# Optimization experiments

Measured on AMD Instinct MI355X. Metric: run time of the kernel, lower is better.

Reference implementation:

```python
import jax, jax.numpy as jnp
import numpy as np
from functools import partial

D_MODEL, N_HEADS, D_FF, KSIZE = 512, 8, 2048, 31
B, S = 8, 1024
EPS = 1e-5

def layer_norm(x, g, b):
    m = jnp.mean(x, axis=-1, keepdims=True)
    v = jnp.mean(jnp.square(x - m), axis=-1, keepdims=True)
    return (x - m) * jax.lax.rsqrt(v + EPS) * g + b

def ffn(x, ln_g, ln_b, w1, b1, w2, b2):
    h = layer_norm(x, ln_g, ln_b)
    h = jax.nn.silu(h @ w1 + b1) @ w2 + b2
    return x + 0.5 * h

def mhsa(x, ln_g, ln_b, wq, bq, wk, bk, wv, bv, wo, bo):
    b_, s_, d_ = x.shape
    dk = d_ // N_HEADS
    h = layer_norm(x, ln_g, ln_b)
    def heads(y):  # (B,S,D) -> (B,H,S,dk)
        return y.reshape(b_, s_, N_HEADS, dk).transpose(0, 2, 1, 3)
    Q, K, V = heads(h @ wq + bq), heads(h @ wk + bk), heads(h @ wv + bv)
    scores = jnp.einsum('bhqd,bhkd->bhqk', Q, K) / jnp.sqrt(jnp.float32(dk)).astype(x.dtype)
    attn = jax.nn.softmax(scores, axis=-1)
    ctx = jnp.einsum('bhqk,bhkd->bhqd', attn, V)
    ctx = ctx.transpose(0, 2, 1, 3).reshape(b_, s_, d_)
    return x + (ctx @ wo + bo)

def conv_module(x, ln_g, ln_b, pw1_w, pw1_b, dw_w, dw_b, bn_g, bn_b, bn_mean, bn_var, pw2_w, pw2_b):
    h = layer_norm(x, ln_g, ln_b)           # (B,S,D)
    h = h @ pw1_w + pw1_b                   # (B,S,2D) pointwise conv1 (k=1)
    a, g = jnp.split(h, 2, axis=-1)
    h = a * jax.nn.sigmoid(g)               # GLU over channel dim
    hc = h.transpose(0, 2, 1)               # (B,D,S)
    # depthwise conv: kernel (D,1,K), groups=D, SAME padding (K odd)
    hc = jax.lax.conv_general_dilated(
        hc, dw_w, window_strides=(1,), padding='SAME',
        dimension_numbers=('NCH', 'OIH', 'NCH'),
        feature_group_count=D_MODEL) + dw_b[None, :, None]
    # BatchNorm1d (eval mode, running stats)
    hc = (hc - bn_mean[None, :, None]) * jax.lax.rsqrt(bn_var + EPS)[None, :, None]
    hc = hc * bn_g[None, :, None] + bn_b[None, :, None]
    hc = jax.nn.silu(hc)
    hc = jnp.einsum('bcs,co->bos', hc, pw2_w) + pw2_b[None, :, None]  # pointwise conv2
    return x + hc.transpose(0, 2, 1)


def setup_inputs() -> dict:
    key = jax.random.key(0)
    ks = iter(jax.random.split(key, 48))
    def w(shape, scale=0.02):
        return (jax.random.normal(next(ks), shape, dtype=jnp.float32) * scale)
    d, f = D_MODEL, D_FF
    inp = {
        'x': jax.random.normal(next(ks), (B, S, d), dtype=jnp.float32),
        # FFN1
        'ffn1_ln_g': jnp.ones((d,)), 'ffn1_ln_b': jnp.zeros((d,)),
        'ffn1_w1': w((d, f)), 'ffn1_b1': jnp.zeros((f,)),
        'ffn1_w2': w((f, d)), 'ffn1_b2': jnp.zeros((d,)),
        # MHSA
        'mhsa_ln_g': jnp.ones((d,)), 'mhsa_ln_b': jnp.zeros((d,)),
        'wq': w((d, d)), 'bq': jnp.zeros((d,)),
        'wk': w((d, d)), 'bk': jnp.zeros((d,)),
        'wv': w((d, d)), 'bv': jnp.zeros((d,)),
        'wo': w((d, d)), 'bo': jnp.zeros((d,)),
        # Conv module
        'conv_ln_g': jnp.ones((d,)), 'conv_ln_b': jnp.zeros((d,)),
        'pw1_w': w((d, 2 * d)), 'pw1_b': jnp.zeros((2 * d,)),
        'dw_w': w((d, 1, KSIZE)), 'dw_b': jnp.zeros((d,)),
        'bn_g': jnp.ones((d,)), 'bn_b': jnp.zeros((d,)),
        'bn_mean': jnp.zeros((d,)), 'bn_var': jnp.ones((d,)),
        'pw2_w': w((d, d)), 'pw2_b': jnp.zeros((d,)),
        # FFN2
        'ffn2_ln_g': jnp.ones((d,)), 'ffn2_ln_b': jnp.zeros((d,)),
        'ffn2_w1': w((d, f)), 'ffn2_b1': jnp.zeros((f,)),
        'ffn2_w2': w((f, d)), 'ffn2_b2': jnp.zeros((d,)),
        # Final LN
        'final_ln_g': jnp.ones((d,)), 'final_ln_b': jnp.zeros((d,)),
    }
    return inp


def reference(x,
              ffn1_ln_g, ffn1_ln_b, ffn1_w1, ffn1_b1, ffn1_w2, ffn1_b2,
              mhsa_ln_g, mhsa_ln_b, wq, bq, wk, bk, wv, bv, wo, bo,
              conv_ln_g, conv_ln_b, pw1_w, pw1_b, dw_w, dw_b,
              bn_g, bn_b, bn_mean, bn_var, pw2_w, pw2_b,
              ffn2_ln_g, ffn2_ln_b, ffn2_w1, ffn2_b1, ffn2_w2, ffn2_b2,
              final_ln_g, final_ln_b):
    h = ffn(x, ffn1_ln_g, ffn1_ln_b, ffn1_w1, ffn1_b1, ffn1_w2, ffn1_b2)
    h = mhsa(h, mhsa_ln_g, mhsa_ln_b, wq, bq, wk, bk, wv, bv, wo, bo)
    h = conv_module(h, conv_ln_g, conv_ln_b, pw1_w, pw1_b, dw_w, dw_b,
                    bn_g, bn_b, bn_mean, bn_var, pw2_w, pw2_b)
    h = ffn(h, ffn2_ln_g, ffn2_ln_b, ffn2_w1, ffn2_b1, ffn2_w2, ffn2_b2)
    return layer_norm(h, final_ln_g, final_ln_b)
```

## Files before the change

### kernel.cpp

```cpp
#include <hip/hip_runtime.h>
#include <hip/hip_bf16.h>
#include <cstddef>

typedef __hip_bfloat16 bf16;
typedef __attribute__((ext_vector_type(8))) short bf16x8;
typedef __attribute__((ext_vector_type(4))) float f32x4;
typedef __attribute__((ext_vector_type(2))) unsigned int u32x2;

static __device__ __forceinline__ float b2f(bf16 v) { return __bfloat162float(v); }
static __device__ __forceinline__ bf16 f2b(float v) { return __float2bfloat16(v); }
static __device__ __forceinline__ float bits2f(unsigned short u) {
    union { unsigned int i; float f; } c; c.i = ((unsigned int)u) << 16; return c.f;
}
static __device__ __forceinline__ unsigned int f2bu(float v) {
    union { bf16 b; unsigned short u; } c; c.b = f2b(v); return (unsigned int)c.u;
}
static __device__ __forceinline__ float ldx(const void* p, size_t i, bool isbf) {
    return isbf ? b2f(((const bf16*)p)[i]) : ((const float*)p)[i];
}
#define GLOAD_LDS16(g, l)                                                            \
    __builtin_amdgcn_global_load_lds((const __attribute__((address_space(1))) unsigned int*)(g), \
                                     (__attribute__((address_space(3))) unsigned int*)(l), 16, 0, 0)

#define LN_EPS 1e-5f

__global__ void detect_kernel(const void* ones, int* flag) {
    unsigned int w = *(const unsigned int*)ones;
    *flag = (w == 0x3F803F80u) ? 1 : 0;
}

__global__ __launch_bounds__(256) void ln_init_kernel(const void* __restrict__ X,
                                                      const void* __restrict__ g,
                                                      const void* __restrict__ b,
                                                      float* __restrict__ res,
                                                      bf16* __restrict__ O, const int* flag) {
    bool isbf = (*flag != 0);
    int tid = threadIdx.x, lane = tid & 63, wid = tid >> 6;
    int t = blockIdx.x * 4 + wid;
    size_t off = (size_t)t * 512 + lane * 8;
    __attribute__((aligned(16))) float v[8];
    if (isbf) {
        bf16x8 xv = *(const bf16x8*)((const bf16*)X + off);
#pragma unroll
        for (int u = 0; u < 8; ++u) v[u] = bits2f((unsigned short)xv[u]);
    } else {
        *(f32x4*)&v[0] = *(const f32x4*)((const float*)X + off);
        *(f32x4*)&v[4] = *(const f32x4*)((const float*)X + off + 4);
    }
    *(f32x4*)(res + off) = *(f32x4*)&v[0];
    *(f32x4*)(res + off + 4) = *(f32x4*)&v[4];
    float s = 0.f, q = 0.f;
#pragma unroll
    for (int u = 0; u < 8; ++u) { s += v[u]; q += v[u] * v[u]; }
#pragma unroll
    for (int m = 1; m < 64; m <<= 1) { s += __shfl_xor(s, m, 64); q += __shfl_xor(q, m, 64); }
    float mean = s * (1.f / 512.f);
    float var  = q * (1.f / 512.f) - mean * mean;
    float sc = rsqrtf(var + LN_EPS);
    __attribute__((aligned(16))) bf16 ov[8];
#pragma unroll
    for (int u = 0; u < 8; ++u)
        ov[u] = f2b((v[u] - mean) * sc * ldx(g, lane * 8 + u, isbf) + ldx(b, lane * 8 + u, isbf));
    *(bf16x8*)(O + off) = *(bf16x8*)ov;
}

__global__ __launch_bounds__(256) void transpose_kernel(const void* __restrict__ W,
                                                        bf16* __restrict__ Wt,
                                                        int K, int M, const int* flag) {
    bool isbf = (*flag != 0);
    __shared__ float ts[32][33];
    int kt0 = blockIdx.x * 32, mt0 = blockIdx.y * 32;
    int x = threadIdx.x, y = threadIdx.y;
    for (int yy = y; yy < 32; yy += 8)
        ts[yy][x] = ldx(W, (size_t)(kt0 + yy) * M + mt0 + x, isbf);
    __syncthreads();
    for (int yy = y; yy < 32; yy += 8)
        Wt[(size_t)(mt0 + yy) * K + kt0 + x] = f2b(ts[x][yy]);
}

__global__ __launch_bounds__(256) void glutrans_kernel(const void* __restrict__ W,
                                                       bf16* __restrict__ Wt, const int* flag) {
    bool isbf = (*flag != 0);
    __shared__ float ts[32][33];
    int kt0 = blockIdx.x * 32, mt0 = blockIdx.y * 32;
    int x = threadIdx.x, y = threadIdx.y;
    for (int yy = y; yy < 32; yy += 8)
        ts[yy][x] = ldx(W, (size_t)(kt0 + yy) * 1024 + mt0 + x, isbf);
    __syncthreads();
    for (int yy = y; yy < 32; yy += 8) {
        int c = mt0 + yy;
        int p = (c < 512) ? (2 * c) : (2 * (c - 512) + 1);
        Wt[(size_t)p * 512 + kt0 + x] = f2b(ts[x][yy]);
    }
}

__global__ void glubias_kernel(const void* __restrict__ b, float* __restrict__ out,
                               const int* flag) {
    bool isbf = (*flag != 0);
    int p = blockIdx.x * blockDim.x + threadIdx.x;
    if (p >= 1024) return;
    int c = (p & 1) ? (p >> 1) + 512 : (p >> 1);
    out[p] = ldx(b, c, isbf);
}

__global__ void bpack_kernel(const void* bq, const void* bk, const void* bv,
                             void* out, const int* flag) {
    bool isbf = (*flag != 0);
    int i = blockIdx.x * blockDim.x + threadIdx.x;
    if (i >= 1536) return;
    const void* src = (i < 512) ? bq : ((i < 1024) ? bk : bv);
    float v = ldx(src, i & 511, isbf);
    if (isbf) ((bf16*)out)[i] = f2b(v);
    else      ((float*)out)[i] = v;
}

__global__ __launch_bounds__(256) void ln_kernel(const float* __restrict__ X,
                                                 const void* __restrict__ g,
                                                 const void* __restrict__ b,
                                                 bf16* __restrict__ O, const int* flag) {
    bool isbf = (*flag != 0);
    int tid = threadIdx.x, lane = tid & 63, wid = tid >> 6;
    int t = blockIdx.x * 4 + wid;
    const float* x = X + (size_t)t * 512 + lane * 8;
    __attribute__((aligned(16))) float v[8];
    *(f32x4*)&v[0] = *(const f32x4*)x;
    *(f32x4*)&v[4] = *(const f32x4*)(x + 4);
    float s = 0.f, q = 0.f;
#pragma unroll
    for (int u = 0; u < 8; ++u) { s += v[u]; q += v[u] * v[u]; }
#pragma unroll
    for (int m = 1; m < 64; m <<= 1) { s += __shfl_xor(s, m, 64); q += __shfl_xor(q, m, 64); }
    float mean = s * (1.f / 512.f);
    float var  = q * (1.f / 512.f) - mean * mean;
    float sc = rsqrtf(var + LN_EPS);
    __attribute__((aligned(16))) bf16 ov[8];
#pragma unroll
    for (int u = 0; u < 8; ++u)
        ov[u] = f2b((v[u] - mean) * sc * ldx(g, lane * 8 + u, isbf) + ldx(b, lane * 8 + u, isbf));
    *(bf16x8*)(O + (size_t)t * 512 + lane * 8) = *(bf16x8*)ov;
}

__global__ __launch_bounds__(256) void ln_out_kernel(const float* __restrict__ X,
                                                     const void* __restrict__ g,
                                                     const void* __restrict__ b,
                                                     void* __restrict__ O, const int* flag) {
    bool isbf = (*flag != 0);
    int tid = threadIdx.x, lane = tid & 63, wid = tid >> 6;
    int t = blockIdx.x * 4 + wid;
    const float* x = X + (size_t)t * 512 + lane * 8;
    __attribute__((aligned(16))) float v[8];
    *(f32x4*)&v[0] = *(const f32x4*)x;
    *(f32x4*)&v[4] = *(const f32x4*)(x + 4);
    float s = 0.f, q = 0.f;
#pragma unroll
    for (int u = 0; u < 8; ++u) { s += v[u]; q += v[u] * v[u]; }
#pragma unroll
    for (int m = 1; m < 64; m <<= 1) { s += __shfl_xor(s, m, 64); q += __shfl_xor(q, m, 64); }
    float mean = s * (1.f / 512.f);
    float var  = q * (1.f / 512.f) - mean * mean;
    float sc = rsqrtf(var + LN_EPS);
    float r[8];
#pragma unroll
    for (int u = 0; u < 8; ++u)
        r[u] = (v[u] - mean) * sc * ldx(g, lane * 8 + u, isbf) + ldx(b, lane * 8 + u, isbf);
    size_t off = (size_t)t * 512 + lane * 8;
    if (isbf) {
        __attribute__((aligned(16))) bf16 ov[8];
#pragma unroll
        for (int u = 0; u < 8; ++u) ov[u] = f2b(r[u]);
        *(bf16x8*)((bf16*)O + off) = *(bf16x8*)ov;
    } else {
        *(f32x4*)((float*)O + off) = *(f32x4*)&r[0];
        *(f32x4*)((float*)O + off + 4) = *(f32x4*)&r[4];
    }
}

template <int ACT, int RESADD, int BM, int MODE>
__global__ __launch_bounds__(256) void mgemm_kernel(const bf16* __restrict__ A,
                                                    const bf16* __restrict__ Wt,
                                                    const void* __restrict__ bias,
                                                    bf16* __restrict__ Cb,
                                                    bf16* __restrict__ vt,
                                                    float* __restrict__ res, float alpha,
                                                    int lda, int K, int M, const int* flag) {
    constexpr int MI = BM / 32;
    bool isbf = (*flag != 0);
    __shared__ short smem[2 * BM * 64 + 2 * 128 * 64];
    short (*As)[BM * 64]  = (short(*)[BM * 64])smem;
    short (*Bs)[128 * 64] = (short(*)[128 * 64])(smem + 2 * BM * 64);
    int tid = threadIdx.x;
    int gx = gridDim.x;
    int nwg = gx * gridDim.y;
    int flat = blockIdx.y * gx + blockIdx.x;
    if ((nwg & 7) == 0) { int cpx = nwg >> 3; flat = (flat & 7) * cpx + (flat >> 3); }
    int rowBase = (flat / gx) * BM, colBase = (flat % gx) * 128;
    int ll = tid & 63, wv = tid >> 6;
    int wr = (wv & 1) * (BM / 2), wc = (wv >> 1) * 64;
    int lRow = ll & 15, quad = ll >> 4;
    int rr = ll >> 3;
    int ch = (ll & 7) ^ rr;
    int slA = (quad ^ (lRow & 7)) * 8;

    int nSteps = K >> 6;

    f32x4 acc[MI][4] = {};

    auto STAGE = [&](int buf, int k0) {
#pragma unroll
        for (int j = 0; j < MI; ++j) {
            int rT = wv * (BM / 4) + j * 8;
            const bf16* ga = A + (size_t)(rowBase + rT + rr) * lda + k0 + ch * 8;
            GLOAD_LDS16(ga, &As[buf][rT * 64]);
        }
#pragma unroll
        for (int j = 0; j < 4; ++j) {
            int rT = wv * 32 + j * 8;
            const bf16* gb = Wt + (size_t)(colBase + rT + rr) * K + k0 + ch * 8;
            GLOAD_LDS16(gb, &Bs[buf][rT * 64]);
        }
    };

    STAGE(0, 0);
    STAGE(1, 64);
    if constexpr (BM == 128) asm volatile("s_waitcnt vmcnt(8)" ::: "memory");
    else                     asm volatile("s_waitcnt vmcnt(6)" ::: "memory");
    __builtin_amdgcn_s_barrier();

    for (int it = 0; it < nSteps; ++it) {
        int cur = it & 1;
        const short* Ac = &As[cur][0];
        const short* Bc = &Bs[cur][0];
        bf16x8 af[2][MI], bfv[2][4];
#pragma unroll
        for (int h = 0; h < 2; ++h) {
            int sl = slA ^ (h * 32);
#pragma unroll
            for (int i = 0; i < MI; ++i)
                af[h][i] = *(const bf16x8*)&Ac[(wr + i * 16 + lRow) * 64 + sl];
#pragma unroll
            for (int j = 0; j < 4; ++j)
                bfv[h][j] = *(const bf16x8*)&Bc[(wc + j * 16 + lRow) * 64 + sl];
        }
        asm volatile("s_waitcnt lgkmcnt(0)" ::: "memory");
        __builtin_amdgcn_s_barrier();
        bool pf = (it + 2 < nSteps);
        if (pf) STAGE(cur, (it + 2) * 64);
#pragma unroll
        for (int h = 0; h < 2; ++h)
#pragma unroll
            for (int i = 0; i < MI; ++i)
#pragma unroll
                for (int j = 0; j < 4; ++j) {
                    if constexpr (MODE == 1)
                        acc[i][j] = __builtin_amdgcn_mfma_f32_16x16x32_bf16(bfv[h][j], af[h][i], acc[i][j], 0, 0, 0);
                    else
                        acc[i][j] = __builtin_amdgcn_mfma_f32_16x16x32_bf16(af[h][i], bfv[h][j], acc[i][j], 0, 0, 0);
                }
        if (pf) {
            if constexpr (BM == 128) asm volatile("s_waitcnt vmcnt(8)" ::: "memory");
            else                     asm volatile("s_waitcnt vmcnt(6)" ::: "memory");
        } else {
            asm volatile("s_waitcnt vmcnt(0)" ::: "memory");
        }
        __builtin_amdgcn_s_barrier();
    }

    if constexpr (MODE == 1) {
        const float* bI = (const float*)bias;
#pragma unroll
        for (int j = 0; j < 4; ++j) {
            int colB = colBase + wc + j * 16 + quad * 4;
            float b0 = bI[colB], b1 = bI[colB + 1], b2 = bI[colB + 2], b3 = bI[colB + 3];
#pragma unroll
            for (int i = 0; i < MI; ++i) {
                int row = rowBase + wr + i * 16 + lRow;
                float a0 = acc[i][j][0] + b0, g0 = acc[i][j][1] + b1;
                float a1 = acc[i][j][2] + b2, g1 = acc[i][j][3] + b3;
                float o0 = a0 / (1.f + __expf(-g0));
                float o1 = a1 / (1.f + __expf(-g1));
                union { bf16 b2_[2]; unsigned int w; } ou;
                ou.b2_[0] = f2b(o0); ou.b2_[1] = f2b(o1);
                *(unsigned int*)(Cb + (size_t)row * (M / 2) + colB / 2) = ou.w;
            }
        }
        return;
    }

    if constexpr (MODE == 2) {
        if (colBase >= 1024) {
            short* T = smem;
#pragma unroll
            for (int j = 0; j < 4; ++j) {
                int colL = wc + j * 16 + lRow;
                float bv = ldx(bias, colBase + colL, isbf);
#pragma unroll
                for (int i = 0; i < MI; ++i) {
                    int r0L = wr + i * 16 + quad * 4;
                    union { bf16 b4[4]; u32x2 w; } ou;
#pragma unroll
                    for (int r = 0; r < 4; ++r) ou.b4[r] = f2b(acc[i][j][r] + bv);
                    *(u32x2*)&T[colL * 136 + r0L] = ou.w;
                }
            }
            __syncthreads();
            int c = tid >> 1, half = tid & 1;
            int cg = colBase - 1024 + c;
            bf16* dst = vt + (size_t)(rowBase >> 10) * 524288 + (size_t)cg * 1024 +
                        (rowBase & 1023) + half * 64;
#pragma unroll
            for (int k = 0; k < 8; ++k)
                *(bf16x8*)(dst + k * 8) = *(const bf16x8*)&T[c * 136 + half * 64 + k * 8];
            return;
        }
    }

#pragma unroll
    for (int j = 0; j < 4; ++j) {
        int col = colBase + wc + j * 16 + lRow;
        float bv = ldx(bias, col, isbf);
#pragma unroll
        for (int i = 0; i < MI; ++i) {
            int r0 = rowBase + wr + i * 16 + quad * 4;
#pragma unroll
            for (int r = 0; r < 4; ++r) {
                float v = acc[i][j][r] + bv;
                if (ACT == 1) v = v / (1.f + __expf(-v));
                int row = r0 + r;
                if (RESADD) res[(size_t)row * 512 + col] += alpha * v;
                else        Cb[(size_t)row * M + col] = f2b(v);
            }
        }
    }
}

__global__ __launch_bounds__(256) void fattn_kernel(bf16* __restrict__ QO,
                                                    const bf16* __restrict__ Vt) {
    __shared__ short Ks[2][64 * 64];
    __shared__ short Vs[2][64 * 64];
    int tid = threadIdx.x, wid = tid >> 6, ll = tid & 63;
    int n = ll & 15, quad = ll >> 4;
    int id = blockIdx.x;
    int ng = gridDim.x >> 3;
    int g = id % ng, j = id / ng;
    int h = g & 7, b = g >> 3;
    size_t rowB = (size_t)b * 1024;
    int q0 = j * 128 + wid * 32;

    const bf16* Qb = QO + rowB * 1536 + h * 64;
    bf16x8 qA0 = *(const bf16x8*)(Qb + (size_t)(q0 + n) * 1536 + quad * 8);
    bf16x8 qA1 = *(const bf16x8*)(Qb + (size_t)(q0 + n) * 1536 + 32 + quad * 8);
    bf16x8 qB0 = *(const bf16x8*)(Qb + (size_t)(q0 + 16 + n) * 1536 + quad * 8);
    bf16x8 qB1 = *(const bf16x8*)(Qb + (size_t)(q0 + 16 + n) * 1536 + 32 + quad * 8);

    const bf16* Kb = QO + rowB * 1536 + 512 + h * 64;
    const bf16* Vb = Vt + (size_t)b * 512 * 1024 + (size_t)(h * 64) * 1024;

    int rr = ll >> 3;
    int ch = (ll & 7) ^ rr;

    float la = 0.f, lb = 0.f;
    f32x4 oaccA0 = {}, oaccA1 = {}, oaccA2 = {}, oaccA3 = {};
    f32x4 oaccB0 = {}, oaccB1 = {}, oaccB2 = {}, oaccB3 = {};
    int idxA = (((quad & 1) * 32) + n) * 4;
    int idxB = idxA + 64;
    bool hiC = (quad >= 2);
    int nx = n & 7;
    int sl0 = (quad ^ nx) * 8;
    int sl1 = sl0 ^ (4 * 8);

    auto STAGE = [&](int buf, int k0) {
#pragma unroll
        for (int i2 = 0; i2 < 2; ++i2) {
            int r0 = wid * 16 + i2 * 8;
            const bf16* gk = Kb + (size_t)(k0 + r0 + rr) * 1536 + ch * 8;
            GLOAD_LDS16(gk, &Ks[buf][r0 * 64]);
            const bf16* gv = Vb + (size_t)(r0 + rr) * 1024 + k0 + ch * 8;
            GLOAD_LDS16(gv, &Vs[buf][r0 * 64]);
        }
    };

    auto COMPUTE = [&](const short* Kc, const short* Vc) {
#pragma unroll
        for (int s = 0; s < 2; ++s) {
            const short* kb0 = Kc + (s * 32 + n) * 64;
            const short* kb1 = kb0 + 16 * 64;
            bf16x8 k00 = *(const bf16x8*)(kb0 + sl0);
            bf16x8 k01 = *(const bf16x8*)(kb0 + sl1);
            bf16x8 k10 = *(const bf16x8*)(kb1 + sl0);
            bf16x8 k11 = *(const bf16x8*)(kb1 + sl1);
            f32x4 sA0 = {}, sA1 = {}, sB0 = {}, sB1 = {};
            sA0 = __builtin_amdgcn_mfma_f32_16x16x32_bf16(k00, qA0, sA0, 0, 0, 0);
            sA0 = __builtin_amdgcn_mfma_f32_16x16x32_bf16(k01, qA1, sA0, 0, 0, 0);
            sA1 = __builtin_amdgcn_mfma_f32_16x16x32_bf16(k10, qA0, sA1, 0, 0, 0);
            sA1 = __builtin_amdgcn_mfma_f32_16x16x32_bf16(k11, qA1, sA1, 0, 0, 0);
            sB0 = __builtin_amdgcn_mfma_f32_16x16x32_bf16(k00, qB0, sB0, 0, 0, 0);
            sB0 = __builtin_amdgcn_mfma_f32_16x16x32_bf16(k01, qB1, sB0, 0, 0, 0);
            sB1 = __builtin_amdgcn_mfma_f32_16x16x32_bf16(k10, qB0, sB1, 0, 0, 0);
            sB1 = __builtin_amdgcn_mfma_f32_16x16x32_bf16(k11, qB1, sB1, 0, 0, 0);

            float pA0[4], pA1[4], pB0[4], pB1[4];
#pragma unroll
            for (int r = 0; r < 4; ++r) {
                pA0[r] = __expf(sA0[r] * 0.125f);
                pA1[r] = __expf(sA1[r] * 0.125f);
                pB0[r] = __expf(sB0[r] * 0.125f);
                pB1[r] = __expf(sB1[r] * 0.125f);
                la += pA0[r] + pA1[r];
                lb += pB0[r] + pB1[r];
            }

            int A0d0 = (int)(f2bu(pA0[0]) | (f2bu(pA0[1]) << 16));
            int A0d1 = (int)(f2bu(pA0[2]) | (f2bu(pA0[3]) << 16));
            int A1d0 = (int)(f2bu(pA1[0]) | (f2bu(pA1[1]) << 16));
            int A1d1 = (int)(f2bu(pA1[2]) | (f2bu(pA1[3]) << 16));
            int B0d0 = (int)(f2bu(pB0[0]) | (f2bu(pB0[1]) << 16));
            int B0d1 = (int)(f2bu(pB0[2]) | (f2bu(pB0[3]) << 16));
            int B1d0 = (int)(f2bu(pB1[0]) | (f2bu(pB1[1]) << 16));
            int B1d1 = (int)(f2bu(pB1[2]) | (f2bu(pB1[3]) << 16));

            int aa0 = __builtin_amdgcn_ds_bpermute(idxA, A0d0);
            int aa1 = __builtin_amdgcn_ds_bpermute(idxA, A0d1);
            int aa2 = __builtin_amdgcn_ds_bpermute(idxB, A0d0);
            int aa3 = __builtin_amdgcn_ds_bpermute(idxB, A0d1);
            int ac0 = __builtin_amdgcn_ds_bpermute(idxA, A1d0);
            int ac1 = __builtin_amdgcn_ds_bpermute(idxA, A1d1);
            int ac2 = __builtin_amdgcn_ds_bpermute(idxB, A1d0);
            int ac3 = __builtin_amdgcn_ds_bpermute(idxB, A1d1);
            int ba0 = __builtin_amdgcn_ds_bpermute(idxA, B0d0);
            int ba1 = __builtin_amdgcn_ds_bpermute(idxA, B0d1);
            int ba2 = __builtin_amdgcn_ds_bpermute(idxB, B0d0);
            int ba3 = __builtin_amdgcn_ds_bpermute(idxB, B0d1);
            int bc0 = __builtin_amdgcn_ds_bpermute(idxA, B1d0);
            int bc1 = __builtin_amdgcn_ds_bpermute(idxA, B1d1);
            int bc2 = __builtin_amdgcn_ds_bpermute(idxB, B1d0);
            int bc3 = __builtin_amdgcn_ds_bpermute(idxB, B1d1);
            union { int d[4]; bf16x8 v; } bfA, bfB;
            bfA.d[0] = hiC ? ac0 : aa0;
            bfA.d[1] = hiC ? ac1 : aa1;
            bfA.d[2] = hiC ? ac2 : aa2;
            bfA.d[3] = hiC ? ac3 : aa3;
            bfB.d[0] = hiC ? bc0 : ba0;
            bfB.d[1] = hiC ? bc1 : ba1;
            bfB.d[2] = hiC ? bc2 : ba2;
            bfB.d[3] = hiC ? bc3 : ba3;

            int vsl = ((s * 4 + quad) ^ nx) * 8;
            bf16x8 v0 = *(const bf16x8*)(Vc + (0 * 16 + n) * 64 + vsl);
            bf16x8 v1 = *(const bf16x8*)(Vc + (1 * 16 + n) * 64 + vsl);
            bf16x8 v2 = *(const bf16x8*)(Vc + (2 * 16 + n) * 64 + vsl);
            bf16x8 v3 = *(const bf16x8*)(Vc + (3 * 16 + n) * 64 + vsl);
            oaccA0 = __builtin_amdgcn_mfma_f32_16x16x32_bf16(v0, bfA.v, oaccA0, 0, 0, 0);
            oaccB0 = __builtin_amdgcn_mfma_f32_16x16x32_bf16(v0, bfB.v, oaccB0, 0, 0, 0);
            oaccA1 = __builtin_amdgcn_mfma_f32_16x16x32_bf16(v1, bfA.v, oaccA1, 0, 0, 0);
            oaccB1 = __builtin_amdgcn_mfma_f32_16x16x32_bf16(v1, bfB.v, oaccB1, 0, 0, 0);
            oaccA2 = __builtin_amdgcn_mfma_f32_16x16x32_bf16(v2, bfA.v, oaccA2, 0, 0, 0);
            oaccB2 = __builtin_amdgcn_mfma_f32_16x16x32_bf16(v2, bfB.v, oaccB2, 0, 0, 0);
            oaccA3 = __builtin_amdgcn_mfma_f32_16x16x32_bf16(v3, bfA.v, oaccA3, 0, 0, 0);
            oaccB3 = __builtin_amdgcn_mfma_f32_16x16x32_bf16(v3, bfB.v, oaccB3, 0, 0, 0);
        }
    };

    STAGE(0, 0);
    __syncthreads();
    for (int it = 0; it < 16; it += 2) {
        if (it + 1 < 16) STAGE(1, (it + 1) * 64);
        COMPUTE(&Ks[0][0], &Vs[0][0]);
        __syncthreads();
        if (it + 2 < 16) STAGE(0, (it + 2) * 64);
        COMPUTE(&Ks[1][0], &Vs[1][0]);
        __syncthreads();
    }

    la += __shfl_xor(la, 16, 64);
    la += __shfl_xor(la, 32, 64);
    lb += __shfl_xor(lb, 16, 64);
    lb += __shfl_xor(lb, 32, 64);
    float linvA = 1.f / la;
    float linvB = 1.f / lb;
    bf16* opA = QO + (rowB + q0 + n) * 1536 + h * 64 + quad * 4;
    bf16* opB = QO + (rowB + q0 + 16 + n) * 1536 + h * 64 + quad * 4;
    {
        union { bf16 b4[4]; u32x2 w; } ou;
#pragma unroll
        for (int r = 0; r < 4; ++r) ou.b4[r] = f2b(oaccA0[r] * linvA);
        *(u32x2*)(opA + 0) = ou.w;
#pragma unroll
        for (int r = 0; r < 4; ++r) ou.b4[r] = f2b(oaccA1[r] * linvA);
        *(u32x2*)(opA + 16) = ou.w;
#pragma unroll
        for (int r = 0; r < 4; ++r) ou.b4[r] = f2b(oaccA2[r] * linvA);
        *(u32x2*)(opA + 32) = ou.w;
#pragma unroll
        for (int r = 0; r < 4; ++r) ou.b4[r] = f2b(oaccA3[r] * linvA);
        *(u32x2*)(opA + 48) = ou.w;
#pragma unroll
        for (int r = 0; r < 4; ++r) ou.b4[r] = f2b(oaccB0[r] * linvB);
        *(u32x2*)(opB + 0) = ou.w;
#pragma unroll
        for (int r = 0; r < 4; ++r) ou.b4[r] = f2b(oaccB1[r] * linvB);
        *(u32x2*)(opB + 16) = ou.w;
#pragma unroll
        for (int r = 0; r < 4; ++r) ou.b4[r] = f2b(oaccB2[r] * linvB);
        *(u32x2*)(opB + 32) = ou.w;
#pragma unroll
        for (int r = 0; r < 4; ++r) ou.b4[r] = f2b(oaccB3[r] * linvB);
        *(u32x2*)(opB + 48) = ou.w;
    }
}

__global__ void dwprep_kernel(const void* __restrict__ w, const void* __restrict__ dwb,
                              const void* __restrict__ bng, const void* __restrict__ bnb,
                              const void* __restrict__ bnm, const void* __restrict__ bnv,
                              bf16* __restrict__ wT, float* __restrict__ scl,
                              float* __restrict__ sft, const int* flag) {
    bool isbf = (*flag != 0);
    int c = blockIdx.x * blockDim.x + threadIdx.x;
    if (c >= 512) return;
    for (int k = 0; k < 31; ++k) wT[k * 512 + c] = f2b(ldx(w, (size_t)c * 31 + k, isbf));
    float s = ldx(bng, c, isbf) * rsqrtf(ldx(bnv, c, isbf) + LN_EPS);
    scl[c] = s;
    sft[c] = (ldx(dwb, c, isbf) - ldx(bnm, c, isbf)) * s + ldx(bnb, c, isbf);
}

__global__ __launch_bounds__(256) void dwconv_kernel(const bf16* __restrict__ X,
                                                     const bf16* __restrict__ wT,
                                                     const float* __restrict__ scl,
                                                     const float* __restrict__ sft,
                                                     bf16* __restrict__ Out) {
    __shared__ bf16 wl[31 * 512];
    __shared__ float sl[512], fl[512];
    int tid = threadIdx.x;
    for (int i = tid; i < (31 * 512) / 8; i += 256)
        *(bf16x8*)&wl[i * 8] = *(const bf16x8*)&wT[i * 8];
    sl[tid] = scl[tid]; sl[tid + 256] = scl[tid + 256];
    fl[tid] = sft[tid]; fl[tid + 256] = sft[tid + 256];
    __syncthreads();

    int lane = tid & 63, sg = tid >> 6;
    int c = lane * 8;
    size_t bOff = (size_t)blockIdx.y * 1024 * 512;
    int sb = blockIdx.x * 16 + sg * 4;

    float acc[4][8] = {};
    for (int kk = 0; kk < 34; ++kk) {
        int sp = sb + kk - 15;
        if (sp < 0 || sp >= 1024) continue;
        bf16x8 xr = *(const bf16x8*)(X + bOff + (size_t)sp * 512 + c);
        float xv[8];
#pragma unroll
        for (int u = 0; u < 8; ++u) xv[u] = bits2f((unsigned short)xr[u]);
#pragma unroll
        for (int o = 0; o < 4; ++o) {
            int kw = kk - o;
            if (kw < 0 || kw > 30) continue;
            bf16x8 wv8 = *(const bf16x8*)&wl[kw * 512 + c];
#pragma unroll
            for (int u = 0; u < 8; ++u) acc[o][u] += xv[u] * bits2f((unsigned short)wv8[u]);
        }
    }
#pragma unroll
    for (int o = 0; o < 4; ++o) {
        __attribute__((aligned(16))) bf16 ov[8];
#pragma unroll
        for (int u = 0; u < 8; ++u) {
            float v = acc[o][u] * sl[c + u] + fl[c + u];
            v = v / (1.f + __expf(-v));
            ov[u] = f2b(v);
        }
        *(bf16x8*)(Out + bOff + (size_t)(sb + o) * 512 + c) = *(bf16x8*)ov;
    }
}

extern "C" void kernel_launch(void* const* d_in, const int* in_sizes, int n_in,
                              void* d_out, int out_size, void* d_ws, size_t ws_size,
                              hipStream_t stream) {
    const int B = 8, S = 1024, D = 512, F = 2048, H = 8;
    const int N = B * S;
    const size_t ND = (size_t)N * D;
    if (n_in < 37) return;

    int idx = 0;
    const void* x          = d_in[idx++];
    const void* ffn1_ln_g  = d_in[idx++];
    const void* ffn1_ln_b  = d_in[idx++];
    const void* ffn1_w1    = d_in[idx++];
    const void* ffn1_b1    = d_in[idx++];
    const void* ffn1_w2    = d_in[idx++];
    const void* ffn1_b2    = d_in[idx++];
    const void* mhsa_ln_g  = d_in[idx++];
    const void* mhsa_ln_b  = d_in[idx++];
    const void* wq         = d_in[idx++];
    const void* bq         = d_in[idx++];
    const void* wk         = d_in[idx++];
    const void* bk         = d_in[idx++];
    const void* wv         = d_in[idx++];
    const void* bv         = d_in[idx++];
    const void* wo         = d_in[idx++];
    const void* bo         = d_in[idx++];
    const void* conv_ln_g  = d_in[idx++];
    const void* conv_ln_b  = d_in[idx++];
    const void* pw1_w      = d_in[idx++];
    const void* pw1_b      = d_in[idx++];
    const void* dw_w       = d_in[idx++];
    const void* dw_b       = d_in[idx++];
    const void* bn_g       = d_in[idx++];
    const void* bn_b       = d_in[idx++];
    const void* bn_mean    = d_in[idx++];
    const void* bn_var     = d_in[idx++];
    const void* pw2_w      = d_in[idx++];
    const void* pw2_b      = d_in[idx++];
    const void* ffn2_ln_g  = d_in[idx++];
    const void* ffn2_ln_b  = d_in[idx++];
    const void* ffn2_w1    = d_in[idx++];
    const void* ffn2_b1    = d_in[idx++];
    const void* ffn2_w2    = d_in[idx++];
    const void* ffn2_b2    = d_in[idx++];
    const void* final_ln_g = d_in[idx++];
    const void* final_ln_b = d_in[idx++];

    const size_t MB = 1024 * 1024;
    char* wsb  = (char*)d_ws;
    int*  flag = (int*)wsb;
    float* res = (float*)(wsb + 1024);
    bf16*  wt  = (bf16*)(wsb + 1024 + ND * 4);
    char*  dwr = wsb + 1024 + ND * 4 + 4 * MB;
    bf16*  dwT  = (bf16*)dwr;
    float* dscl = (float*)(dwr + 32768);
    float* dsft = dscl + 512;
    void*  qkvB = (void*)(dwr + 40960);
    float* gbias = (float*)(dwr + 49152);
    char*  scr = dwr + 65536;
    size_t base = 1024 + ND * 4 + 4 * MB + 65536;
    size_t scrB = (ws_size > base) ? ws_size - base : 0;
    int ffnRows = (scrB >= 32 * MB) ? 8192 : ((scrB >= 8 * MB) ? 2048 : 1024);
    int bI      = (scrB >= 32 * MB) ? 8    : ((scrB >= 8 * MB) ? 2    : 1);
    int cI      = (scrB >= 32 * MB) ? 8    : ((scrB >= 8 * MB) ? 2    : 1);

    bf16* h = (bf16*)d_out;

    detect_kernel<<<1, 1, 0, stream>>>(ffn1_ln_g, flag);
    ln_init_kernel<<<N / 4, 256, 0, stream>>>(x, ffn1_ln_g, ffn1_ln_b, res, h, flag);

    auto run_ffn = [&](const void* lg, const void* lb, const void* w1, const void* b1,
                       const void* w2, const void* b2, bool doLn) {
        bf16* w1t = wt;
        bf16* w2t = wt + (size_t)D * F;
        transpose_kernel<<<dim3(D / 32, F / 32), dim3(32, 8), 0, stream>>>(w1, w1t, D, F, flag);
        transpose_kernel<<<dim3(F / 32, D / 32), dim3(32, 8), 0, stream>>>(w2, w2t, F, D, flag);
        if (doLn) ln_kernel<<<N / 4, 256, 0, stream>>>(res, lg, lb, h, flag);
        bf16* mid = (bf16*)scr;
        for (int r0 = 0; r0 < N; r0 += ffnRows) {
            mgemm_kernel<1, 0, 128, 0><<<dim3(F / 128, ffnRows / 128), 256, 0, stream>>>(
                h + (size_t)r0 * D, w1t, b1, mid, nullptr, nullptr, 0.f, D, D, F, flag);
            mgemm_kernel<0, 1, 64, 0><<<dim3(D / 128, ffnRows / 64), 256, 0, stream>>>(
                mid, w2t, b2, nullptr, nullptr, res + (size_t)r0 * D, 0.5f, F, F, D, flag);
        }
    };

    run_ffn(ffn1_ln_g, ffn1_ln_b, ffn1_w1, ffn1_b1, ffn1_w2, ffn1_b2, false);

    {
        bf16* qt = wt;
        bf16* kt = wt + (size_t)D * D;
        bf16* vt = wt + 2 * (size_t)D * D;
        bf16* ot = wt + 3 * (size_t)D * D;
        transpose_kernel<<<dim3(D / 32, D / 32), dim3(32, 8), 0, stream>>>(wq, qt, D, D, flag);
        transpose_kernel<<<dim3(D / 32, D / 32), dim3(32, 8), 0, stream>>>(wk, kt, D, D, flag);
        transpose_kernel<<<dim3(D / 32, D / 32), dim3(32, 8), 0, stream>>>(wv, vt, D, D, flag);
        transpose_kernel<<<dim3(D / 32, D / 32), dim3(32, 8), 0, stream>>>(wo, ot, D, D, flag);
        bpack_kernel<<<6, 256, 0, stream>>>(bq, bk, bv, qkvB, flag);
        ln_kernel<<<N / 4, 256, 0, stream>>>(res, mhsa_ln_g, mhsa_ln_b, h, flag);
        for (int b = 0; b < B; b += bI) {
            int rows = bI * S;
            bf16* packed = (bf16*)scr;
            bf16* Vt = packed + (size_t)rows * 1536;
            const bf16* Ah = h + (size_t)b * S * D;
            mgemm_kernel<0, 0, 128, 2><<<dim3(1536 / 128, rows / 128), 256, 0, stream>>>(
                Ah, qt, qkvB, packed, Vt, nullptr, 0.f, D, D, 1536, flag);
            fattn_kernel<<<dim3(bI * H * 8), 256, 0, stream>>>(packed, Vt);
            mgemm_kernel<0, 1, 64, 0><<<dim3(D / 128, rows / 64), 256, 0, stream>>>(
                packed, ot, bo, nullptr, nullptr, res + (size_t)b * S * D, 1.0f, 1536, D, D, flag);
        }
    }

    {
        bf16* p1t = wt;
        bf16* p2t = wt + (size_t)D * 2 * D;
        glutrans_kernel<<<dim3(16, 32), dim3(32, 8), 0, stream>>>(pw1_w, p1t, flag);
        glubias_kernel<<<4, 256, 0, stream>>>(pw1_b, gbias, flag);
        transpose_kernel<<<dim3(D / 32, D / 32), dim3(32, 8), 0, stream>>>(pw2_w, p2t, D, D, flag);
        dwprep_kernel<<<2, 256, 0, stream>>>(dw_w, dw_b, bn_g, bn_b, bn_mean, bn_var, dwT, dscl, dsft, flag);
        ln_kernel<<<N / 4, 256, 0, stream>>>(res, conv_ln_g, conv_ln_b, h, flag);
        for (int b = 0; b < B; b += cI) {
            int rows = cI * S;
            bf16* hg = (bf16*)scr;
            bf16* dw = hg + (size_t)rows * D;
            const bf16* Ah = h + (size_t)b * S * D;
            mgemm_kernel<0, 0, 128, 1><<<dim3((2 * D) / 128, rows / 128), 256, 0, stream>>>(
                Ah, p1t, gbias, hg, nullptr, nullptr, 0.f, D, D, 2 * D, flag);
            dwconv_kernel<<<dim3(S / 16, cI), 256, 0, stream>>>(hg, dwT, dscl, dsft, dw);
            mgemm_kernel<0, 1, 64, 0><<<dim3(D / 128, rows / 64), 256, 0, stream>>>(
                dw, p2t, pw2_b, nullptr, nullptr, res + (size_t)b * S * D, 1.0f, D, D, D, flag);
        }
    }

    run_ffn(ffn2_ln_g, ffn2_ln_b, ffn2_w1, ffn2_b1, ffn2_w2, ffn2_b2, true);

    ln_out_kernel<<<N / 4, 256, 0, stream>>>(res, final_ln_g, final_ln_b, d_out, flag);
}
```

Measured before the change: 522.7 us.

## Chunk FFN over hidden dim and shrink QKV scratch stride to fit larger batches

The FFN now loops over chunks of the hidden dimension F across all rows, instead of over row blocks. Each chunk writes a partial result that is accumulated into the residual, and the bias is applied only on the first chunk. The packed QKV buffer drops from a 1536 to a 1024 column stride because V is already written transposed elsewhere. Scratch thresholds are retuned so attention and conv can process more batches per launch. The trade-off is extra read-modify-write passes over the residual, and the first FFN GEMM now uses smaller tiles (BM=64 instead of 128).

```diff
diff --git a/kernel.cpp b/kernel.cpp
--- a/kernel.cpp
+++ b/kernel.cpp
@@ -182,7 +182,8 @@
                                                     bf16* __restrict__ Cb,
                                                     bf16* __restrict__ vt,
                                                     float* __restrict__ res, float alpha,
-                                                    int lda, int K, int M, const int* flag) {
+                                                    int lda, int ldw, int K, int M,
+                                                    int biasOff, float bscale, const int* flag) {
     constexpr int MI = BM / 32;
     bool isbf = (*flag != 0);
     __shared__ short smem[2 * BM * 64 + 2 * 128 * 64];
@@ -215,7 +216,7 @@
 #pragma unroll
         for (int j = 0; j < 4; ++j) {
             int rT = wv * 32 + j * 8;
-            const bf16* gb = Wt + (size_t)(colBase + rT + rr) * K + k0 + ch * 8;
+            const bf16* gb = Wt + (size_t)(colBase + rT + rr) * ldw + k0 + ch * 8;
             GLOAD_LDS16(gb, &Bs[buf][rT * 64]);
         }
     };
@@ -292,7 +293,7 @@
 #pragma unroll
             for (int j = 0; j < 4; ++j) {
                 int colL = wc + j * 16 + lRow;
-                float bv = ldx(bias, colBase + colL, isbf);
+                float bv = ldx(bias, biasOff + colBase + colL, isbf);
 #pragma unroll
                 for (int i = 0; i < MI; ++i) {
                     int r0L = wr + i * 16 + quad * 4;
@@ -317,7 +318,7 @@
 #pragma unroll
     for (int j = 0; j < 4; ++j) {
         int col = colBase + wc + j * 16 + lRow;
-        float bv = ldx(bias, col, isbf);
+        float bv = bscale * ldx(bias, biasOff + col, isbf);
 #pragma unroll
         for (int i = 0; i < MI; ++i) {
             int r0 = rowBase + wr + i * 16 + quad * 4;
@@ -346,13 +347,13 @@
     size_t rowB = (size_t)b * 1024;
     int q0 = j * 128 + wid * 32;
 
-    const bf16* Qb = QO + rowB * 1536 + h * 64;
-    bf16x8 qA0 = *(const bf16x8*)(Qb + (size_t)(q0 + n) * 1536 + quad * 8);
-    bf16x8 qA1 = *(const bf16x8*)(Qb + (size_t)(q0 + n) * 1536 + 32 + quad * 8);
-    bf16x8 qB0 = *(const bf16x8*)(Qb + (size_t)(q0 + 16 + n) * 1536 + quad * 8);
-    bf16x8 qB1 = *(const bf16x8*)(Qb + (size_t)(q0 + 16 + n) * 1536 + 32 + quad * 8);
-
-    const bf16* Kb = QO + rowB * 1536 + 512 + h * 64;
+    const bf16* Qb = QO + rowB * 1024 + h * 64;
+    bf16x8 qA0 = *(const bf16x8*)(Qb + (size_t)(q0 + n) * 1024 + quad * 8);
+    bf16x8 qA1 = *(const bf16x8*)(Qb + (size_t)(q0 + n) * 1024 + 32 + quad * 8);
+    bf16x8 qB0 = *(const bf16x8*)(Qb + (size_t)(q0 + 16 + n) * 1024 + quad * 8);
+    bf16x8 qB1 = *(const bf16x8*)(Qb + (size_t)(q0 + 16 + n) * 1024 + 32 + quad * 8);
+
+    const bf16* Kb = QO + rowB * 1024 + 512 + h * 64;
     const bf16* Vb = Vt + (size_t)b * 512 * 1024 + (size_t)(h * 64) * 1024;
 
     int rr = ll >> 3;
@@ -372,7 +373,7 @@
 #pragma unroll
         for (int i2 = 0; i2 < 2; ++i2) {
             int r0 = wid * 16 + i2 * 8;
-            const bf16* gk = Kb + (size_t)(k0 + r0 + rr) * 1536 + ch * 8;
+            const bf16* gk = Kb + (size_t)(k0 + r0 + rr) * 1024 + ch * 8;
             GLOAD_LDS16(gk, &Ks[buf][r0 * 64]);
             const bf16* gv = Vb + (size_t)(r0 + rr) * 1024 + k0 + ch * 8;
             GLOAD_LDS16(gv, &Vs[buf][r0 * 64]);
@@ -477,8 +478,8 @@
     lb += __shfl_xor(lb, 32, 64);
     float linvA = 1.f / la;
     float linvB = 1.f / lb;
-    bf16* opA = QO + (rowB + q0 + n) * 1536 + h * 64 + quad * 4;
-    bf16* opB = QO + (rowB + q0 + 16 + n) * 1536 + h * 64 + quad * 4;
+    bf16* opA = QO + (rowB + q0 + n) * 1024 + h * 64 + quad * 4;
+    bf16* opB = QO + (rowB + q0 + 16 + n) * 1024 + h * 64 + quad * 4;
     {
         union { bf16 b4[4]; u32x2 w; } ou;
 #pragma unroll
@@ -632,9 +633,9 @@
     char*  scr = dwr + 65536;
     size_t base = 1024 + ND * 4 + 4 * MB + 65536;
     size_t scrB = (ws_size > base) ? ws_size - base : 0;
-    int ffnRows = (scrB >= 32 * MB) ? 8192 : ((scrB >= 8 * MB) ? 2048 : 1024);
-    int bI      = (scrB >= 32 * MB) ? 8    : ((scrB >= 8 * MB) ? 2    : 1);
-    int cI      = (scrB >= 32 * MB) ? 8    : ((scrB >= 8 * MB) ? 2    : 1);
+    int bI = (scrB >= 24 * MB) ? 8 : (scrB >= 12 * MB) ? 4 : (scrB >= 6 * MB) ? 2 : 1;
+    int cI = (scrB >= 16 * MB) ? 8 : (scrB >= 8 * MB) ? 4 : (scrB >= 4 * MB) ? 2 : 1;
+    int FC = (scrB >= 16 * MB) ? 1024 : 512;
 
     bf16* h = (bf16*)d_out;
 
@@ -649,11 +650,13 @@
         transpose_kernel<<<dim3(F / 32, D / 32), dim3(32, 8), 0, stream>>>(w2, w2t, F, D, flag);
         if (doLn) ln_kernel<<<N / 4, 256, 0, stream>>>(res, lg, lb, h, flag);
         bf16* mid = (bf16*)scr;
-        for (int r0 = 0; r0 < N; r0 += ffnRows) {
-            mgemm_kernel<1, 0, 128, 0><<<dim3(F / 128, ffnRows / 128), 256, 0, stream>>>(
-                h + (size_t)r0 * D, w1t, b1, mid, nullptr, nullptr, 0.f, D, D, F, flag);
-            mgemm_kernel<0, 1, 64, 0><<<dim3(D / 128, ffnRows / 64), 256, 0, stream>>>(
-                mid, w2t, b2, nullptr, nullptr, res + (size_t)r0 * D, 0.5f, F, F, D, flag);
+        for (int fc = 0; fc < F / FC; ++fc) {
+            mgemm_kernel<1, 0, 64, 0><<<dim3(FC / 128, N / 64), 256, 0, stream>>>(
+                h, w1t + (size_t)fc * FC * D, b1, mid, nullptr, nullptr, 0.f,
+                D, D, D, FC, fc * FC, 1.f, flag);
+            mgemm_kernel<0, 1, 64, 0><<<dim3(D / 128, N / 64), 256, 0, stream>>>(
+                mid, w2t + (size_t)fc * FC, b2, nullptr, nullptr, res, 0.5f,
+                FC, F, FC, D, 0, (fc == 0) ? 1.f : 0.f, flag);
         }
     };
 
@@ -662,24 +665,25 @@
     {
         bf16* qt = wt;
         bf16* kt = wt + (size_t)D * D;
-        bf16* vt = wt + 2 * (size_t)D * D;
+        bf16* vtw = wt + 2 * (size_t)D * D;
         bf16* ot = wt + 3 * (size_t)D * D;
         transpose_kernel<<<dim3(D / 32, D / 32), dim3(32, 8), 0, stream>>>(wq, qt, D, D, flag);
         transpose_kernel<<<dim3(D / 32, D / 32), dim3(32, 8), 0, stream>>>(wk, kt, D, D, flag);
-        transpose_kernel<<<dim3(D / 32, D / 32), dim3(32, 8), 0, stream>>>(wv, vt, D, D, flag);
+        transpose_kernel<<<dim3(D / 32, D / 32), dim3(32, 8), 0, stream>>>(wv, vtw, D, D, flag);
         transpose_kernel<<<dim3(D / 32, D / 32), dim3(32, 8), 0, stream>>>(wo, ot, D, D, flag);
         bpack_kernel<<<6, 256, 0, stream>>>(bq, bk, bv, qkvB, flag);
         ln_kernel<<<N / 4, 256, 0, stream>>>(res, mhsa_ln_g, mhsa_ln_b, h, flag);
         for (int b = 0; b < B; b += bI) {
             int rows = bI * S;
             bf16* packed = (bf16*)scr;
-            bf16* Vt = packed + (size_t)rows * 1536;
+            bf16* Vt = packed + (size_t)rows * 1024;
             const bf16* Ah = h + (size_t)b * S * D;
             mgemm_kernel<0, 0, 128, 2><<<dim3(1536 / 128, rows / 128), 256, 0, stream>>>(
-                Ah, qt, qkvB, packed, Vt, nullptr, 0.f, D, D, 1536, flag);
+                Ah, qt, qkvB, packed, Vt, nullptr, 0.f, D, D, D, 1024, 0, 1.f, flag);
             fattn_kernel<<<dim3(bI * H * 8), 256, 0, stream>>>(packed, Vt);
             mgemm_kernel<0, 1, 64, 0><<<dim3(D / 128, rows / 64), 256, 0, stream>>>(
-                packed, ot, bo, nullptr, nullptr, res + (size_t)b * S * D, 1.0f, 1536, D, D, flag);
+                packed, ot, bo, nullptr, nullptr, res + (size_t)b * S * D, 1.0f,
+                1024, D, D, D, 0, 1.f, flag);
         }
     }
 
@@ -697,10 +701,11 @@
             bf16* dw = hg + (size_t)rows * D;
             const bf16* Ah = h + (size_t)b * S * D;
             mgemm_kernel<0, 0, 128, 1><<<dim3((2 * D) / 128, rows / 128), 256, 0, stream>>>(
-                Ah, p1t, gbias, hg, nullptr, nullptr, 0.f, D, D, 2 * D, flag);
+                Ah, p1t, gbias, hg, nullptr, nullptr, 0.f, D, D, D, 2 * D, 0, 1.f, flag);
             dwconv_kernel<<<dim3(S / 16, cI), 256, 0, stream>>>(hg, dwT, dscl, dsft, dw);
             mgemm_kernel<0, 1, 64, 0><<<dim3(D / 128, rows / 64), 256, 0, stream>>>(
-                dw, p2t, pw2_b, nullptr, nullptr, res + (size_t)b * S * D, 1.0f, D, D, D, flag);
+                dw, p2t, pw2_b, nullptr, nullptr, res + (size_t)b * S * D, 1.0f,
+                D, D, D, D, 0, 1.f, flag);
         }
     }
 
```

After: 547.1 us. 4.7% more time.
